# Performance work log

Hardware: AMD Instinct MI355X
Metric: run time of the kernel (lower is better)

Reference implementation:

```python
import jax, jax.numpy as jnp
import numpy as np

D_MODEL = 1024
NUM_HEADS = 16
D_KEY = 64
CTX = 2048
B, T = 2, 2048


def setup_inputs() -> dict:
    key = jax.random.key(0)
    ks = jax.random.split(key, 5)
    scale_in = 1.0 / np.sqrt(D_MODEL)
    scale_out = 1.0 / np.sqrt(NUM_HEADS * D_KEY)
    return {
        "X": jax.random.normal(ks[0], (B, T, D_MODEL), dtype=jnp.float32),
        "Wqkv": jax.random.uniform(ks[1], (D_MODEL, 3 * NUM_HEADS * D_KEY), dtype=jnp.float32, minval=-scale_in, maxval=scale_in),
        "bqkv": jax.random.uniform(ks[2], (3 * NUM_HEADS * D_KEY,), dtype=jnp.float32, minval=-scale_in, maxval=scale_in),
        "Wout": jax.random.uniform(ks[3], (NUM_HEADS * D_KEY, D_MODEL), dtype=jnp.float32, minval=-scale_out, maxval=scale_out),
        "bout": jax.random.uniform(ks[4], (D_MODEL,), dtype=jnp.float32, minval=-scale_out, maxval=scale_out),
    }


def reference(X, Wqkv, bqkv, Wout, bout):
    b, t, _ = X.shape
    # project and split into q, k, v: [B,T,3,H,Dk]
    qkv = (X @ Wqkv + bqkv).reshape(b, t, 3, NUM_HEADS, D_KEY)
    q = qkv[:, :, 0].transpose(0, 2, 1, 3)  # [B,H,T,Dk]
    k = qkv[:, :, 1].transpose(0, 2, 1, 3)
    v = qkv[:, :, 2].transpose(0, 2, 1, 3)
    scores = jnp.einsum("bhqd,bhkd->bhqk", q, k) / jnp.sqrt(jnp.float32(D_KEY))
    causal = jnp.tril(jnp.ones((t, t), dtype=bool))  # [T,T]
    scores = jnp.where(causal, scores, -jnp.inf)
    attn = jax.nn.softmax(scores, axis=-1)
    out = jnp.einsum("bhqk,bhkd->bhqd", attn, v)  # [B,H,T,Dk]
    out = out.transpose(0, 2, 1, 3).reshape(b, t, NUM_HEADS * D_KEY)
    return out @ Wout + bout
```

## Files before the change

kernel.cpp:

```cpp
#include <hip/hip_runtime.h>
#include <hip/hip_bf16.h>
#include <math.h>

static constexpr int Bc = 2, Hc = 16, Tc = 2048, DKc = 64, DMc = 1024, NQKV = 3072;
#define QSCALE 0.18033688011112042f

typedef unsigned short u16;
typedef unsigned int u32;
typedef short s8v __attribute__((ext_vector_type(8)));
typedef float f32x4 __attribute__((ext_vector_type(4)));
typedef float f32x16 __attribute__((ext_vector_type(16)));
typedef int i32x4 __attribute__((ext_vector_type(4)));

#define DEVINL __device__ __forceinline__

DEVINL u16 f2b(float f) {
    union { float f; unsigned u; } v; v.f = f;
    unsigned u = v.u;
    unsigned r = (u + 0x7fffu + ((u >> 16) & 1u)) >> 16;
    return (u16)r;
}

DEVINL u32 pkbf16(float lo, float up) {
    u32 r;
    asm volatile("v_cvt_pk_bf16_f32 %0, %1, %2" : "=v"(r) : "v"(lo), "v"(up));
    return r;
}

DEVINL float vexp2(float x) {
    float r;
    asm("v_exp_f32 %0, %1" : "=v"(r) : "v"(x));
    return r;
}

DEVINL void pl32swap(u32& a, u32& b) {
    asm volatile("v_permlane32_swap_b32 %0, %1" : "+v"(a), "+v"(b));
}

DEVINL void gl_lds(const void* g, void* l) {
    __builtin_amdgcn_global_load_lds(
        (const __attribute__((address_space(1))) unsigned int*)g,
        (__attribute__((address_space(3))) unsigned int*)l, 16, 0, 0);
}

DEVINL s8v as_s8v(i32x4 x) { union { i32x4 i; s8v v; } u; u.i = x; return u.v; }

DEVINL void transw_tile(const float* __restrict__ W, u16* __restrict__ Wt,
                        int N, int K, int n0, int k0, u16 (*LT)[72], int t) {
    const int rr = t >> 4, cc = (t & 15) * 4;
    #pragma unroll
    for (int it = 0; it < 4; it++) {
        const int row = it * 16 + rr;
        float4 f = *(const float4*)&W[(size_t)(k0 + row) * N + n0 + cc];
        union { u16 u[4]; uint2 d; } o;
        o.u[0] = f2b(f.x); o.u[1] = f2b(f.y); o.u[2] = f2b(f.z); o.u[3] = f2b(f.w);
        *(uint2*)&LT[row][cc] = o.d;
    }
    __syncthreads();
    #pragma unroll
    for (int it = 0; it < 4; it++) {
        const int nrow = it * 16 + rr;
        union { u16 u[4]; uint2 d; } o;
        #pragma unroll
        for (int j = 0; j < 4; j++) o.u[j] = LT[cc + j][nrow];
        *(uint2*)&Wt[(size_t)(n0 + nrow) * K + k0 + cc] = o.d;
    }
}

__global__ __launch_bounds__(256) void prepass(
    const float* __restrict__ X, u16* __restrict__ Xb,
    const float* __restrict__ Wqkv, u16* __restrict__ Wt1,
    const float* __restrict__ Wout, u16* __restrict__ Wt2)
{
    __shared__ u16 LT[64][72];
    const int bid = blockIdx.x, t = threadIdx.x;
    if (bid < 1024) {
        const int n4 = (Bc * Tc * DMc) / 4;
        for (int i = bid * 256 + t; i < n4; i += 1024 * 256) {
            float4 f = ((const float4*)X)[i];
            union { u16 u[4]; uint2 d; } o;
            o.u[0] = f2b(f.x); o.u[1] = f2b(f.y); o.u[2] = f2b(f.z); o.u[3] = f2b(f.w);
            ((uint2*)Xb)[i] = o.d;
        }
    } else if (bid < 1024 + 768) {
        const int b2 = bid - 1024;
        transw_tile(Wqkv, Wt1, NQKV, DMc, (b2 % 48) * 64, (b2 / 48) * 64, LT, t);
    } else {
        const int b2 = bid - 1792;
        transw_tile(Wout, Wt2, DMc, DMc, (b2 % 16) * 64, (b2 / 16) * 64, LT, t);
    }
}

template <int EPI>
__global__ __launch_bounds__(512) void gemm_cv(
    const u16* __restrict__ A, const u16* __restrict__ Bt,
    const float* __restrict__ bias,
    u16* __restrict__ q_out, u16* __restrict__ k_out, u16* __restrict__ v_out,
    float* __restrict__ f_out, int M, int N, int K, int ntn)
{
    __shared__ __align__(16) u16 Al[2][128 * 32];
    __shared__ __align__(16) u16 Bl[2][128 * 32];
    const int tid = threadIdx.x, lane = tid & 63, w = tid >> 6;
    const int qd = gridDim.x >> 3;
    const int wg = (blockIdx.x & 7) * qd + (blockIdx.x >> 3);
    const int m0 = (wg / ntn) * 128, n0 = (wg % ntn) * 128;
    const int wm = w >> 2, wn = w & 3;

    f32x4 acc[4][2] = {};
    const int nt = K >> 5;

    const int srow = tid >> 2;
    const int skc  = ((tid & 3) ^ ((srow >> 1) & 3)) * 8;

#define STG(t_, s_) do {                                                       \
        const int kk_ = (t_) << 5;                                             \
        gl_lds(A + (size_t)(m0 + srow) * K + kk_ + skc,                        \
               (char*)&Al[s_][0] + w * 1024);                                  \
        gl_lds(Bt + (size_t)(n0 + srow) * K + kk_ + skc,                       \
               (char*)&Bl[s_][0] + w * 1024);                                  \
    } while (0)
#define BARX() do { __builtin_amdgcn_sched_barrier(0);                         \
        __builtin_amdgcn_s_barrier();                                          \
        __builtin_amdgcn_sched_barrier(0); } while (0)

    STG(0, 0);
    int buf = 0;
    for (int t = 0; t < nt; t++) {
        if (t + 1 < nt) {
            STG(t + 1, buf ^ 1);
            asm volatile("s_waitcnt vmcnt(2)" ::: "memory");
        } else {
            asm volatile("s_waitcnt vmcnt(0)" ::: "memory");
        }
        BARX();
        s8v af[4], bf[2];
        #pragma unroll
        for (int mi = 0; mi < 4; mi++) {
            const int row = wm * 64 + mi * 16 + (lane & 15);
            const int slot = (lane >> 4) ^ ((row >> 1) & 3);
            af[mi] = *(const s8v*)((const char*)&Al[buf][0] + row * 64 + slot * 16);
        }
        #pragma unroll
        for (int ni = 0; ni < 2; ni++) {
            const int row = wn * 32 + ni * 16 + (lane & 15);
            const int slot = (lane >> 4) ^ ((row >> 1) & 3);
            bf[ni] = *(const s8v*)((const char*)&Bl[buf][0] + row * 64 + slot * 16);
        }
        #pragma unroll
        for (int mi = 0; mi < 4; mi++)
            #pragma unroll
            for (int ni = 0; ni < 2; ni++)
                acc[mi][ni] = __builtin_amdgcn_mfma_f32_16x16x32_bf16(af[mi], bf[ni], acc[mi][ni], 0, 0, 0);
        BARX();
        buf ^= 1;
    }
#undef STG
#undef BARX

    #pragma unroll
    for (int mi = 0; mi < 4; mi++)
    #pragma unroll
    for (int ni = 0; ni < 2; ni++)
    #pragma unroll
    for (int r = 0; r < 4; r++) {
        const int row = m0 + wm * 64 + mi * 16 + (lane >> 4) * 4 + r;
        const int col = n0 + wn * 32 + ni * 16 + (lane & 15);
        const float val = acc[mi][ni][r] + bias[col];
        if constexpr (EPI == 0) {
            const int sel = col >> 10, rem = col & 1023;
            const int h = rem >> 6, d = rem & 63;
            const int b = row >> 11, tt = row & 2047;
            const size_t idx = ((size_t)(b * Hc + h) * Tc + tt) * DKc + d;
            if (sel == 0) q_out[idx] = f2b(val * QSCALE);
            else if (sel == 1) k_out[idx] = f2b(val);
            else v_out[idx] = f2b(val);
        } else {
            f_out[(size_t)row * N + col] = val;
        }
    }
}

__global__ __launch_bounds__(512) void gemm_n64(
    const u16* __restrict__ A, const u16* __restrict__ Bt,
    const float* __restrict__ bias, float* __restrict__ f_out,
    int M, int N, int K, int ntn)
{
    __shared__ __align__(16) u16 Al[2][128 * 32];
    __shared__ __align__(16) u16 Bl[2][64 * 32];
    const int tid = threadIdx.x, lane = tid & 63, w = tid >> 6;
    const int qd = gridDim.x >> 3;
    const int wg = (blockIdx.x & 7) * qd + (blockIdx.x >> 3);
    const int m0 = (wg / ntn) * 128, n0 = (wg % ntn) * 64;
    const int wm = w >> 1, wn = w & 1;

    f32x4 acc[2][2] = {};
    const int nt = K >> 5;

    const int srow = tid >> 2;
    const int skc  = ((tid & 3) ^ ((srow >> 1) & 3)) * 8;
    const int brow = (tid & 255) >> 2;
    const int bkc  = ((tid & 3) ^ ((brow >> 1) & 3)) * 8;

#define STG(t_, s_) do {                                                       \
        const int kk_ = (t_) << 5;                                             \
        gl_lds(A + (size_t)(m0 + srow) * K + kk_ + skc,                        \
               (char*)&Al[s_][0] + w * 1024);                                  \
        if (w < 4)                                                             \
            gl_lds(Bt + (size_t)(n0 + brow) * K + kk_ + bkc,                   \
                   (char*)&Bl[s_][0] + w * 1024);                              \
    } while (0)
#define BARX() do { __builtin_amdgcn_sched_barrier(0);                         \
        __builtin_amdgcn_s_barrier();                                          \
        __builtin_amdgcn_sched_barrier(0); } while (0)

    STG(0, 0);
    int buf = 0;
    for (int t = 0; t < nt; t++) {
        if (t + 1 < nt) {
            STG(t + 1, buf ^ 1);
            if (w < 4) { asm volatile("s_waitcnt vmcnt(2)" ::: "memory"); }
            else       { asm volatile("s_waitcnt vmcnt(1)" ::: "memory"); }
        } else {
            asm volatile("s_waitcnt vmcnt(0)" ::: "memory");
        }
        BARX();
        s8v af[2], bf[2];
        #pragma unroll
        for (int mi = 0; mi < 2; mi++) {
            const int row = wm * 32 + mi * 16 + (lane & 15);
            const int slot = (lane >> 4) ^ ((row >> 1) & 3);
            af[mi] = *(const s8v*)((const char*)&Al[buf][0] + row * 64 + slot * 16);
        }
        #pragma unroll
        for (int ni = 0; ni < 2; ni++) {
            const int row = wn * 32 + ni * 16 + (lane & 15);
            const int slot = (lane >> 4) ^ ((row >> 1) & 3);
            bf[ni] = *(const s8v*)((const char*)&Bl[buf][0] + row * 64 + slot * 16);
        }
        #pragma unroll
        for (int mi = 0; mi < 2; mi++)
            #pragma unroll
            for (int ni = 0; ni < 2; ni++)
                acc[mi][ni] = __builtin_amdgcn_mfma_f32_16x16x32_bf16(af[mi], bf[ni], acc[mi][ni], 0, 0, 0);
        BARX();
        buf ^= 1;
    }
#undef STG
#undef BARX

    #pragma unroll
    for (int mi = 0; mi < 2; mi++)
    #pragma unroll
    for (int ni = 0; ni < 2; ni++)
    #pragma unroll
    for (int r = 0; r < 4; r++) {
        const int row = m0 + wm * 32 + mi * 16 + (lane >> 4) * 4 + r;
        const int col = n0 + wn * 32 + ni * 16 + (lane & 15);
        f_out[(size_t)row * N + col] = acc[mi][ni][r] + bias[col];
    }
}

__global__ __launch_bounds__(512) void attn_fwd(
    const u16* __restrict__ Q, const u16* __restrict__ K,
    const u16* __restrict__ V, u16* __restrict__ O)
{
    __shared__ __align__(16) char Gl[2][2][2][8192];

    const int bid = blockIdx.x;
    const int bh = bid & 31;
    const int qt = 15 - (bid >> 5);
    const int tid = threadIdx.x;
    const int g = tid >> 8;
    const int gtid = tid & 255;
    const int lane = tid & 63;
    const int ws = (tid >> 6) & 3;
    const int hi = lane >> 5, lq = lane & 31;
    const int q0w = qt * 128 + ws * 32;
    const int qg = q0w + lq;

    const u16* Qb = Q + (size_t)bh * (Tc * DKc);
    const u16* Kb = K + (size_t)bh * (Tc * DKc);
    const u16* Vb = V + (size_t)bh * (Tc * DKc);

    s8v qf[4];
    #pragma unroll
    for (int st = 0; st < 4; st++)
        qf[st] = *(const s8v*)(Qb + (size_t)qg * 64 + st * 16 + hi * 8);

    f32x16 o0 = {}, o1 = {}, lacc = {};

    const int dtw = (q0w + 31) >> 6;
    const int h = qt + 1;
    const int t0 = g * h;

    char* const Kbase = &Gl[g][0][0][0];
    char* const Vbase = &Gl[g][1][0][0];

    const int d2 = (gtid & 31) * 2, kb8 = gtid >> 5;
    const unsigned vsw0 = ((unsigned)(d2 & 7)) << 4;
    const unsigned vsw1 = ((unsigned)((d2 + 1) & 7)) << 4;
    const unsigned ksw = ((unsigned)(lq & 7)) << 4;

    u32 vx[8];

#define ISSUE_K(kt_, dst_) do {                                              \
        const char* Ktile_ = (const char*)(Kb + (size_t)(kt_) * 4096);       \
        _Pragma("unroll")                                                    \
        for (int s_ = 0; s_ < 2; s_++) {                                     \
            const int o_ = s_ * 4096 + gtid * 16;                            \
            const int rk_ = o_ >> 7;                                         \
            const int cb_ = (o_ & 127) ^ ((rk_ & 7) << 4);                   \
            gl_lds(Ktile_ + rk_ * 128 + cb_, (dst_) + s_ * 4096 + ws * 1024); \
        }                                                                    \
    } while (0)

#define LOAD_V(kt_) do {                                                     \
        const u16* Vtile_ = Vb + (size_t)(kt_) * 4096;                       \
        _Pragma("unroll")                                                    \
        for (int i_ = 0; i_ < 8; i_++)                                       \
            vx[i_] = *(const u32*)(Vtile_ + (kb8 * 8 + i_) * 64 + d2);       \
    } while (0)

#define WRITE_V(dst_) do {                                                   \
        s8v v0_, v1_;                                                        \
        _Pragma("unroll")                                                    \
        for (int i_ = 0; i_ < 8; i_++) {                                     \
            v0_[i_] = (short)(vx[i_] & 0xffff);                              \
            v1_[i_] = (short)(vx[i_] >> 16);                                 \
        }                                                                    \
        *(s8v*)((dst_) + d2 * 128 + (((unsigned)(kb8 * 16)) ^ vsw0)) = v0_;  \
        *(s8v*)((dst_) + (d2 + 1) * 128 + (((unsigned)(kb8 * 16)) ^ vsw1)) = v1_; \
    } while (0)

    ISSUE_K(t0, Kbase);
    LOAD_V(t0);
    WRITE_V(Vbase);
    __syncthreads();

    int c = 0;
    for (int i = 0; i < h; i++) {
        const int tki = t0 + i;
        const bool pf_next = (i + 1 < h);
        if (pf_next) {
            ISSUE_K(tki + 1, Kbase + (c ^ 1) * 8192);
            LOAD_V(tki + 1);
        }

        if (tki <= dtw) {
            const char* Kc = Kbase + c * 8192;
            const char* Vc = Vbase + c * 8192;
            f32x16 s0v = {}, s1v = {};
            __builtin_amdgcn_s_setprio(1);
            #pragma unroll
            for (int st = 0; st < 4; st++) {
                const unsigned cbs = (unsigned)(st * 32 + hi * 16);
                s8v kf0 = *(const s8v*)(Kc + lq * 128 + (cbs ^ ksw));
                s8v kf1 = *(const s8v*)(Kc + (32 + lq) * 128 + (cbs ^ ksw));
                s0v = __builtin_amdgcn_mfma_f32_32x32x16_bf16(kf0, qf[st], s0v, 0, 0, 0);
                s1v = __builtin_amdgcn_mfma_f32_32x32x16_bf16(kf1, qf[st], s1v, 0, 0, 0);
            }
            __builtin_amdgcn_s_setprio(0);

            if (tki == dtw) {
                #pragma unroll
                for (int r = 0; r < 16; r++) {
                    const int kg = tki * 64 + (r & 3) + 8 * (r >> 2) + 4 * hi;
                    if (kg > qg) s0v[r] = -INFINITY;
                    if (kg + 32 > qg) s1v[r] = -INFINITY;
                }
            }

            #pragma unroll
            for (int r = 0; r < 16; r++) {
                s0v[r] = vexp2(s0v[r]);
                s1v[r] = vexp2(s1v[r]);
            }
            lacc += s0v;
            lacc += s1v;

            i32x4 pf[4];
            #pragma unroll
            for (int gq = 0; gq < 2; gq++) {
                #pragma unroll
                for (int hq = 0; hq < 2; hq++) {
                    const int base = hq * 8;
                    u32 a0, a1, b0, b1;
                    if (gq == 0) {
                        a0 = pkbf16(s0v[base + 0], s0v[base + 1]);
                        a1 = pkbf16(s0v[base + 2], s0v[base + 3]);
                        b0 = pkbf16(s0v[base + 4], s0v[base + 5]);
                        b1 = pkbf16(s0v[base + 6], s0v[base + 7]);
                    } else {
                        a0 = pkbf16(s1v[base + 0], s1v[base + 1]);
                        a1 = pkbf16(s1v[base + 2], s1v[base + 3]);
                        b0 = pkbf16(s1v[base + 4], s1v[base + 5]);
                        b1 = pkbf16(s1v[base + 6], s1v[base + 7]);
                    }
                    pl32swap(a0, b0);
                    pl32swap(a1, b1);
                    pf[gq * 2 + hq][0] = (int)a0;
                    pf[gq * 2 + hq][1] = (int)a1;
                    pf[gq * 2 + hq][2] = (int)b0;
                    pf[gq * 2 + hq][3] = (int)b1;
                }
            }

            __builtin_amdgcn_s_setprio(1);
            #pragma unroll
            for (int ks = 0; ks < 4; ks++) {
                const unsigned cbv = (unsigned)(ks * 32 + hi * 16);
                s8v vf0 = *(const s8v*)(Vc + lq * 128 + (cbv ^ ksw));
                s8v vf1 = *(const s8v*)(Vc + (32 + lq) * 128 + (cbv ^ ksw));
                const s8v pa = as_s8v(pf[ks]);
                o0 = __builtin_amdgcn_mfma_f32_32x32x16_bf16(pa, vf0, o0, 0, 0, 0);
                o1 = __builtin_amdgcn_mfma_f32_32x32x16_bf16(pa, vf1, o1, 0, 0, 0);
            }
            __builtin_amdgcn_s_setprio(0);
        }

        if (pf_next) WRITE_V(Vbase + (c ^ 1) * 8192);
        __syncthreads();
        c ^= 1;
    }

    float t8[8];
    #pragma unroll
    for (int r = 0; r < 8; r++) t8[r] = lacc[r] + lacc[r + 8];
    #pragma unroll
    for (int off = 4; off >= 1; off >>= 1)
        #pragma unroll
        for (int r = 0; r < off; r++) t8[r] = t8[r] + t8[r + off];
    float ls = t8[0] + __shfl_xor(t8[0], 32);

    float* Pf = (float*)(&Gl[0][0][0][0]) + ws * 2304;
    if (g == 1) {
        float* dst = Pf + lane * 34;
        #pragma unroll
        for (int r = 0; r < 16; r++) { dst[r] = o0[r]; dst[16 + r] = o1[r]; }
        Pf[2176 + lane] = ls;
    }
    __syncthreads();
    if (g == 0) {
        const float* src = Pf + lane * 34;
        #pragma unroll
        for (int r = 0; r < 16; r++) { o0[r] += src[r]; o1[r] += src[16 + r]; }
        ls += Pf[2176 + lane];

        const float linv = 1.0f / ls;
        const int b = bh >> 4, hh = bh & 15;
        u16* Ob = O + ((size_t)b * Tc) * DMc + hh * 64;
        #pragma unroll
        for (int r = 0; r < 16; r++) {
            const int cr = (r & 3) + 8 * (r >> 2) + 4 * hi;
            const float ir = __shfl(linv, cr);
            u16* orow = Ob + (size_t)(q0w + cr) * DMc;
            orow[lq]      = f2b(o0[r] * ir);
            orow[32 + lq] = f2b(o1[r] * ir);
        }
    }
#undef ISSUE_K
#undef LOAD_V
#undef WRITE_V
}

extern "C" void kernel_launch(void* const* d_in, const int* in_sizes, int n_in,
                              void* d_out, int out_size, void* d_ws, size_t ws_size,
                              hipStream_t stream)
{
    const float* X    = (const float*)d_in[0];
    const float* Wqkv = (const float*)d_in[1];
    const float* bqkv = (const float*)d_in[2];
    const float* Wout = (const float*)d_in[3];
    const float* bout = (const float*)d_in[4];
    float* out = (float*)d_out;

    char* ws = (char*)d_ws;
    u16* Xb  = (u16*)(ws);
    u16* Ow  = (u16*)(ws);
    u16* Wt1 = (u16*)(ws + (8 << 20));
    u16* Wt2 = (u16*)(ws + (14 << 20));
    u16* Qw  = (u16*)(ws + (16 << 20));
    u16* Kw  = (u16*)(ws + (24 << 20));
    u16* Vw  = (u16*)(ws + (32 << 20));

    prepass<<<2048, 256, 0, stream>>>(X, Xb, Wqkv, Wt1, Wout, Wt2);

    gemm_cv<0><<<768, 512, 0, stream>>>(
        Xb, Wt1, bqkv, Qw, Kw, Vw, nullptr, Bc * Tc, NQKV, DMc, NQKV / 128);

    attn_fwd<<<512, 512, 0, stream>>>(Qw, Kw, Vw, Ow);

    gemm_n64<<<512, 512, 0, stream>>>(
        Ow, Wt2, bout, out, Bc * Tc, DMc, DMc, DMc / 64);
}
```

Baseline: 97.24 us.

## Fuse X fp32-to-bf16 conversion into QKV GEMM A-tile loading

```diff
diff --git a/kernel.cpp b/kernel.cpp
--- a/kernel.cpp
+++ b/kernel.cpp
@@ -68,35 +68,24 @@
 }
 
 __global__ __launch_bounds__(256) void prepass(
-    const float* __restrict__ X, u16* __restrict__ Xb,
     const float* __restrict__ Wqkv, u16* __restrict__ Wt1,
     const float* __restrict__ Wout, u16* __restrict__ Wt2)
 {
     __shared__ u16 LT[64][72];
     const int bid = blockIdx.x, t = threadIdx.x;
-    if (bid < 1024) {
-        const int n4 = (Bc * Tc * DMc) / 4;
-        for (int i = bid * 256 + t; i < n4; i += 1024 * 256) {
-            float4 f = ((const float4*)X)[i];
-            union { u16 u[4]; uint2 d; } o;
-            o.u[0] = f2b(f.x); o.u[1] = f2b(f.y); o.u[2] = f2b(f.z); o.u[3] = f2b(f.w);
-            ((uint2*)Xb)[i] = o.d;
-        }
-    } else if (bid < 1024 + 768) {
-        const int b2 = bid - 1024;
-        transw_tile(Wqkv, Wt1, NQKV, DMc, (b2 % 48) * 64, (b2 / 48) * 64, LT, t);
+    if (bid < 768) {
+        transw_tile(Wqkv, Wt1, NQKV, DMc, (bid % 48) * 64, (bid / 48) * 64, LT, t);
     } else {
-        const int b2 = bid - 1792;
+        const int b2 = bid - 768;
         transw_tile(Wout, Wt2, DMc, DMc, (b2 % 16) * 64, (b2 / 16) * 64, LT, t);
     }
 }
 
-template <int EPI>
-__global__ __launch_bounds__(512) void gemm_cv(
-    const u16* __restrict__ A, const u16* __restrict__ Bt,
+__global__ __launch_bounds__(512) void gemm_xf(
+    const float* __restrict__ X, const u16* __restrict__ Bt,
     const float* __restrict__ bias,
     u16* __restrict__ q_out, u16* __restrict__ k_out, u16* __restrict__ v_out,
-    float* __restrict__ f_out, int M, int N, int K, int ntn)
+    int M, int N, int K, int ntn)
 {
     __shared__ __align__(16) u16 Al[2][128 * 32];
     __shared__ __align__(16) u16 Bl[2][128 * 32];
@@ -111,24 +100,40 @@
 
     const int srow = tid >> 2;
     const int skc  = ((tid & 3) ^ ((srow >> 1) & 3)) * 8;
-
-#define STG(t_, s_) do {                                                       \
-        const int kk_ = (t_) << 5;                                             \
-        gl_lds(A + (size_t)(m0 + srow) * K + kk_ + skc,                        \
-               (char*)&Al[s_][0] + w * 1024);                                  \
-        gl_lds(Bt + (size_t)(n0 + srow) * K + kk_ + skc,                       \
-               (char*)&Bl[s_][0] + w * 1024);                                  \
+    const float* xrow = X + (size_t)(m0 + srow) * K + skc;
+
+    float4 a0v, a1v;
+
+#define ALOAD(t_) do {                                                         \
+        a0v = *(const float4*)(xrow + ((t_) << 5));                            \
+        a1v = *(const float4*)(xrow + ((t_) << 5) + 4);                        \
     } while (0)
+#define AWRITE(s_) do {                                                        \
+        i32x4 wv_;                                                             \
+        wv_[0] = (int)pkbf16(a0v.x, a0v.y);                                    \
+        wv_[1] = (int)pkbf16(a0v.z, a0v.w);                                    \
+        wv_[2] = (int)pkbf16(a1v.x, a1v.y);                                    \
+        wv_[3] = (int)pkbf16(a1v.z, a1v.w);                                    \
+        *(i32x4*)((char*)&Al[s_][0] + tid * 16) = wv_;                         \
+    } while (0)
+#define BSTG(t_, s_) gl_lds(Bt + (size_t)(n0 + srow) * K + ((t_) << 5) + skc,  \
+                            (char*)&Bl[s_][0] + w * 1024)
 #define BARX() do { __builtin_amdgcn_sched_barrier(0);                         \
         __builtin_amdgcn_s_barrier();                                          \
         __builtin_amdgcn_sched_barrier(0); } while (0)
 
-    STG(0, 0);
+    ALOAD(0);
+    BSTG(0, 0);
+    asm volatile("s_waitcnt vmcnt(1)" ::: "memory");
+    AWRITE(0);
+    asm volatile("s_waitcnt lgkmcnt(0)" ::: "memory");
+
     int buf = 0;
     for (int t = 0; t < nt; t++) {
         if (t + 1 < nt) {
-            STG(t + 1, buf ^ 1);
-            asm volatile("s_waitcnt vmcnt(2)" ::: "memory");
+            ALOAD(t + 1);
+            BSTG(t + 1, buf ^ 1);
+            asm volatile("s_waitcnt vmcnt(3)" ::: "memory");
         } else {
             asm volatile("s_waitcnt vmcnt(0)" ::: "memory");
         }
@@ -151,10 +156,17 @@
             #pragma unroll
             for (int ni = 0; ni < 2; ni++)
                 acc[mi][ni] = __builtin_amdgcn_mfma_f32_16x16x32_bf16(af[mi], bf[ni], acc[mi][ni], 0, 0, 0);
+        if (t + 1 < nt) {
+            asm volatile("s_waitcnt vmcnt(1)" ::: "memory");
+            AWRITE(buf ^ 1);
+            asm volatile("s_waitcnt lgkmcnt(0)" ::: "memory");
+        }
         BARX();
         buf ^= 1;
     }
-#undef STG
+#undef ALOAD
+#undef AWRITE
+#undef BSTG
 #undef BARX
 
     #pragma unroll
@@ -166,17 +178,13 @@
         const int row = m0 + wm * 64 + mi * 16 + (lane >> 4) * 4 + r;
         const int col = n0 + wn * 32 + ni * 16 + (lane & 15);
         const float val = acc[mi][ni][r] + bias[col];
-        if constexpr (EPI == 0) {
-            const int sel = col >> 10, rem = col & 1023;
-            const int h = rem >> 6, d = rem & 63;
-            const int b = row >> 11, tt = row & 2047;
-            const size_t idx = ((size_t)(b * Hc + h) * Tc + tt) * DKc + d;
-            if (sel == 0) q_out[idx] = f2b(val * QSCALE);
-            else if (sel == 1) k_out[idx] = f2b(val);
-            else v_out[idx] = f2b(val);
-        } else {
-            f_out[(size_t)row * N + col] = val;
-        }
+        const int sel = col >> 10, rem = col & 1023;
+        const int h = rem >> 6, d = rem & 63;
+        const int b = row >> 11, tt = row & 2047;
+        const size_t idx = ((size_t)(b * Hc + h) * Tc + tt) * DKc + d;
+        if (sel == 0) q_out[idx] = f2b(val * QSCALE);
+        else if (sel == 1) k_out[idx] = f2b(val);
+        else v_out[idx] = f2b(val);
     }
 }
 
@@ -475,7 +483,6 @@
     float* out = (float*)d_out;
 
     char* ws = (char*)d_ws;
-    u16* Xb  = (u16*)(ws);
     u16* Ow  = (u16*)(ws);
     u16* Wt1 = (u16*)(ws + (8 << 20));
     u16* Wt2 = (u16*)(ws + (14 << 20));
@@ -483,10 +490,10 @@
     u16* Kw  = (u16*)(ws + (24 << 20));
     u16* Vw  = (u16*)(ws + (32 << 20));
 
-    prepass<<<2048, 256, 0, stream>>>(X, Xb, Wqkv, Wt1, Wout, Wt2);
-
-    gemm_cv<0><<<768, 512, 0, stream>>>(
-        Xb, Wt1, bqkv, Qw, Kw, Vw, nullptr, Bc * Tc, NQKV, DMc, NQKV / 128);
+    prepass<<<1024, 256, 0, stream>>>(Wqkv, Wt1, Wout, Wt2);
+
+    gemm_xf<<<768, 512, 0, stream>>>(
+        X, Wt1, bqkv, Qw, Kw, Vw, Bc * Tc, NQKV, DMc, NQKV / 128);
 
     attn_fwd<<<512, 512, 0, stream>>>(Qw, Kw, Vw, Ow);
 
```

After: 98.78 us. Within noise of the previous version (+1.6%).
